# Kernel optimization log

Measured on AMD Instinct MI355X. Metric: run time of the kernel, lower is better.

The kernel has to match this reference:

```python
import jax, jax.numpy as jnp
import numpy as np

S, B, N, H = 64, 32, 325, 64

def setup_inputs() -> dict:
    key = jax.random.key(0)
    k1, k2, k3, k4 = jax.random.split(key, 4)
    return {
        "encoder_outputs": jax.random.normal(k1, (S, B, N, H), dtype=jnp.float32),
        "decoder_hidden": jax.random.normal(k2, (B, N, H), dtype=jnp.float32),
        "W": jax.random.normal(k3, (H, H), dtype=jnp.float32) * (1.0 / np.sqrt(H)),
        "b": jax.random.normal(k4, (H,), dtype=jnp.float32) * 0.01,
    }

def reference(encoder_outputs, decoder_hidden, W, b):
    # energy: (S,B,N,H) -- Linear + tanh
    energy = jnp.tanh(jnp.einsum('sbnh,kh->sbnk', encoder_outputs, W) + b)
    # broadcast multiply by decoder_hidden (B,N,H) and reduce over hidden dim -> (S,B,N)
    e = jnp.einsum('sbnh,bnh->sbn', energy, decoder_hidden)
    # softmax over seq_len, output (B,N,S)
    return jax.nn.softmax(jnp.transpose(e, (1, 2, 0)), axis=-1)
```

## Files before the change

### kernel.cpp

```cpp
#include <hip/hip_runtime.h>


constexpr int S = 64, B = 32, N = 325, H = 64;
constexpr int BN = B * N;

typedef __attribute__((ext_vector_type(8))) short short8;
typedef __attribute__((ext_vector_type(4))) float f32x4;

union FragU { unsigned u[4]; short8 s8; uint4 v4; };

__device__ inline unsigned pack_hi(float x0, float x1, float& r0, float& r1) {
    unsigned u0 = __builtin_bit_cast(unsigned, x0);
    unsigned u1 = __builtin_bit_cast(unsigned, x1);
    r0 = x0 - __builtin_bit_cast(float, u0 & 0xffff0000u);
    r1 = x1 - __builtin_bit_cast(float, u1 & 0xffff0000u);
    return (u0 >> 16) | (u1 & 0xffff0000u);
}
__device__ inline unsigned pack_bf(float x0, float x1) {
    return (__builtin_bit_cast(unsigned, x0) >> 16) |
           (__builtin_bit_cast(unsigned, x1) & 0xffff0000u);
}

__global__ void pack_w(const float* __restrict__ W, uint4* __restrict__ wp) {
    int idx  = blockIdx.x * blockDim.x + threadIdx.x;
    if (idx >= 512) return;
    int q    = idx >> 7;
    int kc   = (idx >> 6) & 1;
    int lane = idx & 63;
    int col  = lane & 15, grp = lane >> 4;
    const float4* wpt = (const float4*)(W + (q * 16 + col) * H + kc * 32 + grp * 8);
    float4 w0 = wpt[0], w1 = wpt[1];
    float r0, r1, r2, r3, r4, r5, r6, r7;
    FragU hi, lo;
    hi.u[0] = pack_hi(w0.x, w0.y, r0, r1);
    hi.u[1] = pack_hi(w0.z, w0.w, r2, r3);
    hi.u[2] = pack_hi(w1.x, w1.y, r4, r5);
    hi.u[3] = pack_hi(w1.z, w1.w, r6, r7);
    lo.u[0] = pack_bf(r0, r1);
    lo.u[1] = pack_bf(r2, r3);
    lo.u[2] = pack_bf(r4, r5);
    lo.u[3] = pack_bf(r6, r7);
    wp[((q * 2 + kc) * 2 + 0) * 64 + lane] = hi.v4;
    wp[((q * 2 + kc) * 2 + 1) * 64 + lane] = lo.v4;
}

__global__ __launch_bounds__(256) void attn_mfma2(
    const float* __restrict__ enc,
    const float* __restrict__ dec,
    const float* __restrict__ bias,
    const uint4* __restrict__ wp,
    float* __restrict__ out)
{
    const int lane  = threadIdx.x & 63;
    const int wv    = threadIdx.x >> 6;
    const int bnl   = wv >> 1;
    const int shalf = wv & 1;
    const int bn    = blockIdx.x * 2 + bnl;
    const int col   = lane & 15;
    const int grp   = lane >> 4;

    __shared__ float P[4][16 * 33];
    __shared__ float eS[2][64];
    float* Pw = P[wv];

    float bias_v[4], dec_v[4];
#pragma unroll
    for (int q = 0; q < 4; ++q) {
        bias_v[q] = bias[q * 16 + col];
        dec_v[q]  = dec[bn * H + q * 16 + col];
    }

    FragU a_hi[2][2], a_lo[2][2];
#pragma unroll
    for (int mt = 0; mt < 2; ++mt) {
        const float* er = enc + (((shalf * 2 + mt) * 16 + col) * BN + bn) * H;
#pragma unroll
        for (int kc = 0; kc < 2; ++kc) {
            const float4* p4 = (const float4*)(er + kc * 32 + grp * 8);
            float4 x0 = p4[0], x1 = p4[1];
            float r0, r1, r2, r3, r4, r5, r6, r7;
            a_hi[mt][kc].u[0] = pack_hi(x0.x, x0.y, r0, r1);
            a_hi[mt][kc].u[1] = pack_hi(x0.z, x0.w, r2, r3);
            a_hi[mt][kc].u[2] = pack_hi(x1.x, x1.y, r4, r5);
            a_hi[mt][kc].u[3] = pack_hi(x1.z, x1.w, r6, r7);
            a_lo[mt][kc].u[0] = pack_bf(r0, r1);
            a_lo[mt][kc].u[1] = pack_bf(r2, r3);
            a_lo[mt][kc].u[2] = pack_bf(r4, r5);
            a_lo[mt][kc].u[3] = pack_bf(r6, r7);
        }
    }

    float e_s = 0.0f;
#pragma unroll
    for (int q = 0; q < 4; ++q) {
        f32x4 acc[2];
#pragma unroll
        for (int mt = 0; mt < 2; ++mt) acc[mt] = (f32x4){0.f, 0.f, 0.f, 0.f};

#pragma unroll
        for (int kc = 0; kc < 2; ++kc) {
            FragU bh, bl;
            bh.v4 = wp[((q * 2 + kc) * 2 + 0) * 64 + lane];
            bl.v4 = wp[((q * 2 + kc) * 2 + 1) * 64 + lane];
#pragma unroll
            for (int mt = 0; mt < 2; ++mt) {
                acc[mt] = __builtin_amdgcn_mfma_f32_16x16x32_bf16(a_hi[mt][kc].s8, bh.s8, acc[mt], 0, 0, 0);
                acc[mt] = __builtin_amdgcn_mfma_f32_16x16x32_bf16(a_lo[mt][kc].s8, bh.s8, acc[mt], 0, 0, 0);
                acc[mt] = __builtin_amdgcn_mfma_f32_16x16x32_bf16(a_hi[mt][kc].s8, bl.s8, acc[mt], 0, 0, 0);
            }
        }

#pragma unroll
        for (int mt = 0; mt < 2; ++mt) {
#pragma unroll
            for (int r = 0; r < 4; ++r) {
                int sl  = mt * 16 + grp * 4 + r;
                float a = acc[mt][r] + bias_v[q];
                float t = 1.0f - 2.0f * __builtin_amdgcn_rcpf(__expf(2.0f * a) + 1.0f);
                Pw[col * 33 + sl] = t * dec_v[q];
            }
        }
#pragma unroll
        for (int k = 0; k < 16; ++k)
            e_s += Pw[k * 33 + (lane & 31)];
    }

    if (lane < 32) eS[bnl][shalf * 32 + lane] = e_s;
    __syncthreads();
    float ev = eS[bnl][lane];

    float m = ev;
#pragma unroll
    for (int off = 32; off > 0; off >>= 1)
        m = fmaxf(m, __shfl_xor(m, off, 64));
    float p = __expf(ev - m);
    float sum = p;
#pragma unroll
    for (int off = 32; off > 0; off >>= 1)
        sum += __shfl_xor(sum, off, 64);

    if (shalf == 0)
        out[bn * S + lane] = p * __builtin_amdgcn_rcpf(sum);
}

extern "C" void kernel_launch(void* const* d_in, const int* in_sizes, int n_in,
                              void* d_out, int out_size, void* d_ws, size_t ws_size,
                              hipStream_t stream) {
    const float* enc  = (const float*)d_in[0];
    const float* dec  = (const float*)d_in[1];
    const float* W    = (const float*)d_in[2];
    const float* bias = (const float*)d_in[3];
    float* out        = (float*)d_out;

    pack_w<<<2, 256, 0, stream>>>(W, (uint4*)d_ws);
    attn_mfma2<<<BN / 2, 256, 0, stream>>>(enc, dec, bias, (const uint4*)d_ws, out);
}
```

Before: 257.9 us.

## Split fused attention into contiguous-row energy kernel and separate softmax kernel

```diff
diff --git a/kernel.cpp b/kernel.cpp
--- a/kernel.cpp
+++ b/kernel.cpp
@@ -3,6 +3,7 @@
 
 constexpr int S = 64, B = 32, N = 325, H = 64;
 constexpr int BN = B * N;
+constexpr int SBN = S * BN;
 
 typedef __attribute__((ext_vector_type(8))) short short8;
 typedef __attribute__((ext_vector_type(4))) float f32x4;
@@ -22,12 +23,10 @@
 }
 
 __global__ void pack_w(const float* __restrict__ W, uint4* __restrict__ wp) {
-    int idx  = blockIdx.x * blockDim.x + threadIdx.x;
+    int idx = blockIdx.x * blockDim.x + threadIdx.x;
     if (idx >= 512) return;
-    int q    = idx >> 7;
-    int kc   = (idx >> 6) & 1;
-    int lane = idx & 63;
-    int col  = lane & 15, grp = lane >> 4;
+    int q = idx >> 7, kc = (idx >> 6) & 1, lane = idx & 63;
+    int col = lane & 15, grp = lane >> 4;
     const float4* wpt = (const float4*)(W + (q * 16 + col) * H + kc * 32 + grp * 8);
     float4 w0 = wpt[0], w1 = wpt[1];
     float r0, r1, r2, r3, r4, r5, r6, r7;
@@ -36,44 +35,26 @@
     hi.u[1] = pack_hi(w0.z, w0.w, r2, r3);
     hi.u[2] = pack_hi(w1.x, w1.y, r4, r5);
     hi.u[3] = pack_hi(w1.z, w1.w, r6, r7);
-    lo.u[0] = pack_bf(r0, r1);
-    lo.u[1] = pack_bf(r2, r3);
-    lo.u[2] = pack_bf(r4, r5);
-    lo.u[3] = pack_bf(r6, r7);
+    lo.u[0] = pack_bf(r0, r1); lo.u[1] = pack_bf(r2, r3);
+    lo.u[2] = pack_bf(r4, r5); lo.u[3] = pack_bf(r6, r7);
     wp[((q * 2 + kc) * 2 + 0) * 64 + lane] = hi.v4;
     wp[((q * 2 + kc) * 2 + 1) * 64 + lane] = lo.v4;
 }
 
-__global__ __launch_bounds__(256) void attn_mfma2(
-    const float* __restrict__ enc,
-    const float* __restrict__ dec,
-    const float* __restrict__ bias,
-    const uint4* __restrict__ wp,
-    float* __restrict__ out)
+__global__ __launch_bounds__(256) void energy_k(
+    const float* __restrict__ enc, const float* __restrict__ dec,
+    const float* __restrict__ bias, const uint4* __restrict__ wp,
+    float* __restrict__ e)
 {
-    const int lane  = threadIdx.x & 63;
-    const int wv    = threadIdx.x >> 6;
-    const int bnl   = wv >> 1;
-    const int shalf = wv & 1;
-    const int bn    = blockIdx.x * 2 + bnl;
-    const int col   = lane & 15;
-    const int grp   = lane >> 4;
-
-    __shared__ float P[4][16 * 33];
-    __shared__ float eS[2][64];
-    float* Pw = P[wv];
-
-    float bias_v[4], dec_v[4];
-#pragma unroll
-    for (int q = 0; q < 4; ++q) {
-        bias_v[q] = bias[q * 16 + col];
-        dec_v[q]  = dec[bn * H + q * 16 + col];
-    }
+    const int lane = threadIdx.x & 63;
+    const int wv   = threadIdx.x >> 6;
+    const int col  = lane & 15, grp = lane >> 4;
+    const int row0 = (blockIdx.x * 4 + wv) * 32;
 
     FragU a_hi[2][2], a_lo[2][2];
 #pragma unroll
     for (int mt = 0; mt < 2; ++mt) {
-        const float* er = enc + (((shalf * 2 + mt) * 16 + col) * BN + bn) * H;
+        const float* er = enc + (row0 + mt * 16 + col) * H;
 #pragma unroll
         for (int kc = 0; kc < 2; ++kc) {
             const float4* p4 = (const float4*)(er + kc * 32 + grp * 8);
@@ -90,13 +71,31 @@
         }
     }
 
-    float e_s = 0.0f;
+    int doff[2][4];
+#pragma unroll
+    for (int mt = 0; mt < 2; ++mt)
+#pragma unroll
+        for (int r = 0; r < 4; ++r) {
+            unsigned sbn = (unsigned)(row0 + mt * 16 + grp * 4 + r);
+            unsigned bn  = sbn % (unsigned)BN;
+            doff[mt][r]  = (int)(bn * H) + col;
+        }
+
+    float bias_v[4];
+#pragma unroll
+    for (int q = 0; q < 4; ++q) bias_v[q] = bias[q * 16 + col];
+
+    float part[2][4];
+#pragma unroll
+    for (int mt = 0; mt < 2; ++mt)
+#pragma unroll
+        for (int r = 0; r < 4; ++r) part[mt][r] = 0.0f;
+
 #pragma unroll
     for (int q = 0; q < 4; ++q) {
         f32x4 acc[2];
-#pragma unroll
-        for (int mt = 0; mt < 2; ++mt) acc[mt] = (f32x4){0.f, 0.f, 0.f, 0.f};
-
+        acc[0] = (f32x4){0.f, 0.f, 0.f, 0.f};
+        acc[1] = (f32x4){0.f, 0.f, 0.f, 0.f};
 #pragma unroll
         for (int kc = 0; kc < 2; ++kc) {
             FragU bh, bl;
@@ -109,38 +108,95 @@
                 acc[mt] = __builtin_amdgcn_mfma_f32_16x16x32_bf16(a_hi[mt][kc].s8, bl.s8, acc[mt], 0, 0, 0);
             }
         }
-
-#pragma unroll
-        for (int mt = 0; mt < 2; ++mt) {
+#pragma unroll
+        for (int mt = 0; mt < 2; ++mt)
 #pragma unroll
             for (int r = 0; r < 4; ++r) {
-                int sl  = mt * 16 + grp * 4 + r;
                 float a = acc[mt][r] + bias_v[q];
                 float t = 1.0f - 2.0f * __builtin_amdgcn_rcpf(__expf(2.0f * a) + 1.0f);
-                Pw[col * 33 + sl] = t * dec_v[q];
+                part[mt][r] = fmaf(t, dec[doff[mt][r] + q * 16], part[mt][r]);
             }
-        }
-#pragma unroll
-        for (int k = 0; k < 16; ++k)
-            e_s += Pw[k * 33 + (lane & 31)];
-    }
-
-    if (lane < 32) eS[bnl][shalf * 32 + lane] = e_s;
-    __syncthreads();
-    float ev = eS[bnl][lane];
-
-    float m = ev;
-#pragma unroll
-    for (int off = 32; off > 0; off >>= 1)
-        m = fmaxf(m, __shfl_xor(m, off, 64));
-    float p = __expf(ev - m);
-    float sum = p;
-#pragma unroll
-    for (int off = 32; off > 0; off >>= 1)
-        sum += __shfl_xor(sum, off, 64);
-
-    if (shalf == 0)
-        out[bn * S + lane] = p * __builtin_amdgcn_rcpf(sum);
+    }
+
+#pragma unroll
+    for (int mt = 0; mt < 2; ++mt)
+#pragma unroll
+        for (int r = 0; r < 4; ++r) {
+            float v = part[mt][r];
+            v += __shfl_xor(v, 1, 64);
+            v += __shfl_xor(v, 2, 64);
+            v += __shfl_xor(v, 4, 64);
+            v += __shfl_xor(v, 8, 64);
+            part[mt][r] = v;
+        }
+
+    float va = (col & 1) ? part[0][1] : part[0][0];
+    float vb = (col & 1) ? part[0][3] : part[0][2];
+    float vc = (col & 1) ? part[1][1] : part[1][0];
+    float vd = (col & 1) ? part[1][3] : part[1][2];
+    float ve = (col & 2) ? vb : va;
+    float vf = (col & 2) ? vd : vc;
+    float vo = (col & 4) ? vf : ve;
+    if (col < 8)
+        e[row0 + ((col >> 2) & 1) * 16 + grp * 4 + (col & 3)] = vo;
+}
+
+__global__ __launch_bounds__(256) void softmax_k(
+    const float* __restrict__ e,
+    float* __restrict__ out)
+{
+    __shared__ float Et[64 * 65];
+    __shared__ float Mred[4][64], Sred[4][64], Mfin[64], Rfin[64];
+
+    const int t = threadIdx.x;
+    const int bn0 = blockIdx.x * 64;
+    const int lane = t & 63, w = t >> 6;
+
+#pragma unroll
+    for (int i = 0; i < 16; ++i) {
+        int s = w * 16 + i;
+        float v = (bn0 + lane < BN) ? e[s * BN + bn0 + lane] : 0.0f;
+        Et[s * 65 + lane] = v;
+    }
+    __syncthreads();
+
+    {
+        const int bn_loc = t & 63, sq = t >> 6;
+        float m = -1e30f;
+#pragma unroll
+        for (int i = 0; i < 16; ++i)
+            m = fmaxf(m, Et[(sq * 16 + i) * 65 + bn_loc]);
+        Mred[sq][bn_loc] = m;
+    }
+    __syncthreads();
+    {
+        const int bn_loc = t & 63, sq = t >> 6;
+        float m = fmaxf(fmaxf(Mred[0][bn_loc], Mred[1][bn_loc]),
+                        fmaxf(Mred[2][bn_loc], Mred[3][bn_loc]));
+        float sum = 0.0f;
+#pragma unroll
+        for (int i = 0; i < 16; ++i)
+            sum += __expf(Et[(sq * 16 + i) * 65 + bn_loc] - m);
+        Sred[sq][bn_loc] = sum;
+        if (sq == 0) Mfin[bn_loc] = m;
+    }
+    __syncthreads();
+    if ((t >> 6) == 0) {
+        const int bn_loc = t & 63;
+        float sum = Sred[0][bn_loc] + Sred[1][bn_loc] + Sred[2][bn_loc] + Sred[3][bn_loc];
+        Rfin[bn_loc] = __builtin_amdgcn_rcpf(sum);
+    }
+    __syncthreads();
+
+    const int s_out = t & 63, bq = t >> 6;
+#pragma unroll
+    for (int j = 0; j < 16; ++j) {
+        int bn_loc = bq * 16 + j;
+        if (bn0 + bn_loc < BN) {
+            float p = __expf(Et[s_out * 65 + bn_loc] - Mfin[bn_loc]) * Rfin[bn_loc];
+            out[(bn0 + bn_loc) * S + s_out] = p;
+        }
+    }
 }
 
 extern "C" void kernel_launch(void* const* d_in, const int* in_sizes, int n_in,
@@ -152,6 +208,10 @@
     const float* bias = (const float*)d_in[3];
     float* out        = (float*)d_out;
 
-    pack_w<<<2, 256, 0, stream>>>(W, (uint4*)d_ws);
-    attn_mfma2<<<BN / 2, 256, 0, stream>>>(enc, dec, bias, (const uint4*)d_ws, out);
-}
+    uint4* wp = (uint4*)d_ws;
+    float* e  = (float*)((char*)d_ws + 65536);
+
+    pack_w<<<2, 256, 0, stream>>>(W, wp);
+    energy_k<<<SBN / 128, 256, 0, stream>>>(enc, dec, bias, wp, e);
+    softmax_k<<<(BN + 63) / 64, 256, 0, stream>>>(e, out);
+}
```

Result: no change. 254.8 us (-1.2%).
